# Optimization experiments

Hardware: AMD Instinct MI355X
Metric: run time of the kernel (lower is better)

## Reference

```python
import jax, jax.numpy as jnp
import numpy as np
import math

B, L, OBS, ACT = 2, 1024, 64, 16
OE, AE, RE, TE = 512, 256, 128, 128
C, H, NL, FF = 1024, 16, 4, 4096
DH = C // H


def setup_inputs():
    key = jax.random.key(0)
    ks = jax.random.split(key, 20)
    def nrm(k, shape, std=1.0):
        return jax.random.normal(k, shape, jnp.float32) * std
    kb = jax.random.split(ks[19], 12)
    return {
        'obs_seq': nrm(ks[0], (B, L, OBS)),
        'act_seq': nrm(ks[1], (B, L, ACT)),
        'rew_seq': nrm(ks[2], (B, L, 1)),
        'obs_W': nrm(ks[3], (OBS, OE), OBS ** -0.5), 'obs_b': jnp.zeros((OE,)),
        'act_W': nrm(ks[4], (ACT, AE), ACT ** -0.5), 'act_b': jnp.zeros((AE,)),
        'rew_W': nrm(ks[5], (1, RE), 1.0), 'rew_b': jnp.zeros((RE,)),
        'tr_W': nrm(ks[6], (OBS, TE), OBS ** -0.5), 'tr_b': jnp.zeros((TE,)),
        'bn_gamma': jnp.ones((OBS,)), 'bn_beta': jnp.zeros((OBS,)),
        'ln1_w': jnp.ones((NL, C)), 'ln1_b': jnp.zeros((NL, C)),
        'qkv_W': nrm(kb[0], (NL, C, 3 * C), C ** -0.5), 'qkv_b': jnp.zeros((NL, 3 * C)),
        'out_W': nrm(kb[1], (NL, C, C), C ** -0.5), 'out_b': jnp.zeros((NL, C)),
        'ln2_w': jnp.ones((NL, C)), 'ln2_b': jnp.zeros((NL, C)),
        'fc_W': nrm(kb[2], (NL, C, FF), C ** -0.5), 'fc_b': jnp.zeros((NL, FF)),
        'pj_W': nrm(kb[3], (NL, FF, C), FF ** -0.5), 'pj_b': jnp.zeros((NL, C)),
    }


def _ln(x, w, b):
    m = x.mean(-1, keepdims=True)
    v = ((x - m) ** 2).mean(-1, keepdims=True)
    return (x - m) * jax.lax.rsqrt(v + 1e-5) * w + b


def _forward(obs_seq, act_seq, rew_seq, obs_W, obs_b, act_W, act_b, rew_W, rew_b,
             tr_W, tr_b, bn_gamma, bn_beta, ln1_w, ln1_b, qkv_W, qkv_b, out_W, out_b,
             ln2_w, ln2_b, fc_W, fc_b, pj_W, pj_b):
    # transition branch: prepend first obs, take deltas; BatchNorm1d in training
    # mode uses biased batch stats over (batch, time) per channel.
    full_obs = jnp.concatenate([obs_seq[:, :1], obs_seq], axis=1)  # (B, L+1, OBS)
    obs2 = full_obs[:, :-1]
    tran = full_obs[:, 1:] - full_obs[:, :-1]  # (B, L, OBS)
    tm = tran.mean((0, 1))
    tv = ((tran - tm) ** 2).mean((0, 1))
    tran = (tran - tm) * jax.lax.rsqrt(tv + 1e-5) * bn_gamma + bn_beta
    # encoder_activation is identity
    enc = jnp.concatenate([
        obs2 @ obs_W + obs_b,
        act_seq @ act_W + act_b,
        rew_seq @ rew_W + rew_b,
        tran @ tr_W + tr_b,
    ], axis=-1)  # (B, L, C)
    mask = jnp.tril(jnp.ones((L, L), dtype=bool))

    def block(x, p):
        l1w, l1b, qW, qb, oW, ob, l2w, l2b, fW, fb, pW, pb = p
        h = _ln(x, l1w, l1b)
        q, k, v = jnp.split(h @ qW + qb, 3, axis=-1)
        q, k, v = (t.reshape(B, L, H, DH).transpose(0, 2, 1, 3) for t in (q, k, v))
        s = jnp.einsum('bhqd,bhkd->bhqk', q, k) / math.sqrt(DH)
        s = jnp.where(mask, s, -jnp.inf)
        a = jax.nn.softmax(s, axis=-1)
        o = jnp.einsum('bhqk,bhkd->bhqd', a, v).transpose(0, 2, 1, 3).reshape(B, L, C)
        x = x + o @ oW + ob  # residual + out_proj
        h2 = _ln(x, l2w, l2b)
        x = x + jax.nn.relu(h2 @ fW + fb) @ pW + pb  # MLP residual
        return x, None

    x, _ = jax.lax.scan(block, enc, (ln1_w, ln1_b, qkv_W, qkv_b, out_W, out_b,
                                     ln2_w, ln2_b, fc_W, fc_b, pj_W, pj_b))
    return jnp.tanh(x)


def reference(obs_seq, act_seq, rew_seq, obs_W, obs_b, act_W, act_b, rew_W, rew_b,
              tr_W, tr_b, bn_gamma, bn_beta, ln1_w, ln1_b, qkv_W, qkv_b, out_W, out_b,
              ln2_w, ln2_b, fc_W, fc_b, pj_W, pj_b):
    return _forward(obs_seq, act_seq, rew_seq, obs_W, obs_b, act_W, act_b, rew_W, rew_b,
                    tr_W, tr_b, bn_gamma, bn_beta, ln1_w, ln1_b, qkv_W, qkv_b, out_W, out_b,
                    ln2_w, ln2_b, fc_W, fc_b, pj_W, pj_b)
```

## Files before the change

kernel.cpp:

```cpp
#include <hip/hip_runtime.h>
#include <hip/hip_bf16.h>
#include <math.h>

constexpr int kB   = 2;
constexpr int kL   = 1024;
constexpr int kOBS = 64;
constexpr int kACT = 16;
constexpr int kC   = 1024;
constexpr int kH   = 16;
constexpr int kDH  = 64;
constexpr int kFF  = 4096;
constexpr int kNL  = 4;
constexpr int kRows = kB * kL;
constexpr int kOE = 512, kAE = 256, kRE = 128, kTE = 128;

typedef _Float16 f16x8 __attribute__((ext_vector_type(8)));
typedef _Float16 f16x4 __attribute__((ext_vector_type(4)));
typedef float    f32x4 __attribute__((ext_vector_type(4)));

__device__ __forceinline__ unsigned short f2h(float x) {
    return __builtin_bit_cast(unsigned short, (_Float16)x);
}
__device__ __forceinline__ void gload_lds16(const void* g, void* l) {
    __builtin_amdgcn_global_load_lds(
        (const __attribute__((address_space(1))) unsigned int*)g,
        (__attribute__((address_space(3))) unsigned int*)l, 16, 0, 0);
}

__global__ __launch_bounds__(256) void tran_stats_kernel(
    const float* __restrict__ obs, float* __restrict__ tm, float* __restrict__ tv)
{
    const int f = blockIdx.x;
    const int tid = threadIdx.x;
    float sum = 0.f, sq = 0.f;
    for (int r = tid; r < kRows; r += 256) {
        const int t = r & (kL - 1);
        float d = 0.f;
        if (t > 0) {
            const float cur  = obs[(size_t)r * kOBS + f];
            const float prev = obs[(size_t)(r - 1) * kOBS + f];
            d = cur - prev;
        }
        sum += d; sq += d * d;
    }
    for (int off = 32; off > 0; off >>= 1) {
        sum += __shfl_down(sum, off);
        sq  += __shfl_down(sq, off);
    }
    __shared__ float sa[4], sb[4];
    if ((tid & 63) == 0) { sa[tid >> 6] = sum; sb[tid >> 6] = sq; }
    __syncthreads();
    if (tid == 0) {
        const float ts = sa[0] + sa[1] + sa[2] + sa[3];
        const float tq = sb[0] + sb[1] + sb[2] + sb[3];
        const float m = ts / (float)kRows;
        tm[f] = m;
        tv[f] = tq / (float)kRows - m * m;
    }
}

__global__ __launch_bounds__(256) void encode_kernel(
    const float* __restrict__ obs, const float* __restrict__ act, const float* __restrict__ rew,
    const float* __restrict__ obs_W, const float* __restrict__ obs_b,
    const float* __restrict__ act_W, const float* __restrict__ act_b,
    const float* __restrict__ rew_W, const float* __restrict__ rew_b,
    const float* __restrict__ tr_W,  const float* __restrict__ tr_b,
    const float* __restrict__ bn_g,  const float* __restrict__ bn_b,
    const float* __restrict__ tm,    const float* __restrict__ tv,
    float* __restrict__ enc)
{
    const int row = blockIdx.x;
    const int t = row & (kL - 1);
    const int tid = threadIdx.x;
    __shared__ float s_obs2[kOBS];
    __shared__ float s_tran[kOBS];
    __shared__ float s_act[kACT];
    __shared__ float s_rew;
    if (tid < kOBS) {
        const float cur  = obs[(size_t)row * kOBS + tid];
        const float prev = (t > 0) ? obs[(size_t)(row - 1) * kOBS + tid] : cur;
        s_obs2[tid] = prev;
        const float tr = cur - prev;
        s_tran[tid] = (tr - tm[tid]) * rsqrtf(tv[tid] + 1e-5f) * bn_g[tid] + bn_b[tid];
    } else if (tid < kOBS + kACT) {
        s_act[tid - kOBS] = act[(size_t)row * kACT + (tid - kOBS)];
    } else if (tid == kOBS + kACT) {
        s_rew = rew[row];
    }
    __syncthreads();
    float* er = enc + (size_t)row * kC;
    #pragma unroll
    for (int s = 0; s < 4; ++s) {
        const int c = tid + s * 256;
        float v;
        if (c < kOE) {
            v = obs_b[c];
            #pragma unroll
            for (int k = 0; k < kOBS; ++k) v += s_obs2[k] * obs_W[k * kOE + c];
        } else if (c < kOE + kAE) {
            const int cc = c - kOE;
            v = act_b[cc];
            #pragma unroll
            for (int k = 0; k < kACT; ++k) v += s_act[k] * act_W[k * kAE + cc];
        } else if (c < kOE + kAE + kRE) {
            const int cc = c - (kOE + kAE);
            v = s_rew * rew_W[cc] + rew_b[cc];
        } else {
            const int cc = c - (kOE + kAE + kRE);
            v = tr_b[cc];
            #pragma unroll
            for (int k = 0; k < kOBS; ++k) v += s_tran[k] * tr_W[k * kTE + cc];
        }
        er[c] = v;
    }
}

__global__ __launch_bounds__(256) void ln_kernel(
    const float* __restrict__ x, const float* __restrict__ w,
    const float* __restrict__ b, unsigned short* __restrict__ out)
{
    const int row = blockIdx.x;
    const int tid = threadIdx.x;
    const float4 xv = *reinterpret_cast<const float4*>(&x[(size_t)row * kC + tid * 4]);
    float s = xv.x + xv.y + xv.z + xv.w;
    float q = xv.x * xv.x + xv.y * xv.y + xv.z * xv.z + xv.w * xv.w;
    for (int off = 32; off > 0; off >>= 1) {
        s += __shfl_down(s, off);
        q += __shfl_down(q, off);
    }
    __shared__ float sa[4], sb[4];
    if ((tid & 63) == 0) { sa[tid >> 6] = s; sb[tid >> 6] = q; }
    __syncthreads();
    const float ts = sa[0] + sa[1] + sa[2] + sa[3];
    const float tq = sb[0] + sb[1] + sb[2] + sb[3];
    const float mean = ts * (1.f / kC);
    const float var  = tq * (1.f / kC) - mean * mean;
    const float rstd = rsqrtf(var + 1e-5f);
    const float4 wv = *reinterpret_cast<const float4*>(&w[tid * 4]);
    const float4 bv = *reinterpret_cast<const float4*>(&b[tid * 4]);
    ushort4 o;
    o.x = f2h((xv.x - mean) * rstd * wv.x + bv.x);
    o.y = f2h((xv.y - mean) * rstd * wv.y + bv.y);
    o.z = f2h((xv.z - mean) * rstd * wv.z + bv.z);
    o.w = f2h((xv.w - mean) * rstd * wv.w + bv.w);
    *reinterpret_cast<ushort4*>(&out[(size_t)row * kC + tid * 4]) = o;
}

__device__ __forceinline__ void convT_tile(
    const float* __restrict__ W, unsigned short* __restrict__ WT,
    int K, int N, int k0, int n0, int tid)
{
    __shared__ unsigned short t[64][68];
    const int r = tid >> 4, c4 = (tid & 15) * 4;
    #pragma unroll
    for (int s = 0; s < 4; ++s) {
        const int rr = r + s * 16;
        const float4 v = *reinterpret_cast<const float4*>(&W[(size_t)(k0 + rr) * N + n0 + c4]);
        t[rr][c4 + 0] = f2h(v.x);
        t[rr][c4 + 1] = f2h(v.y);
        t[rr][c4 + 2] = f2h(v.z);
        t[rr][c4 + 3] = f2h(v.w);
    }
    __syncthreads();
    #pragma unroll
    for (int s = 0; s < 4; ++s) {
        const int rn = r + s * 16;
        ushort4 o;
        o.x = t[c4 + 0][rn];
        o.y = t[c4 + 1][rn];
        o.z = t[c4 + 2][rn];
        o.w = t[c4 + 3][rn];
        *reinterpret_cast<ushort4*>(&WT[(size_t)(n0 + rn) * K + k0 + c4]) = o;
    }
}

__global__ __launch_bounds__(256) void convert_layer_kernel(
    const float* __restrict__ qW, const float* __restrict__ oW,
    const float* __restrict__ fW, const float* __restrict__ pW,
    unsigned short* __restrict__ qWT, unsigned short* __restrict__ oWT,
    unsigned short* __restrict__ fWT, unsigned short* __restrict__ pWT)
{
    int bid = blockIdx.x;
    const int tid = threadIdx.x;
    if (bid < 768)  {
        convT_tile(qW, qWT, 1024, 3072, (bid / 48) * 64, (bid % 48) * 64, tid);
    } else if (bid < 1024) {
        bid -= 768;
        convT_tile(oW, oWT, 1024, 1024, (bid / 16) * 64, (bid % 16) * 64, tid);
    } else if (bid < 2048) {
        bid -= 1024;
        convT_tile(fW, fWT, 1024, 4096, (bid / 64) * 64, (bid % 64) * 64, tid);
    } else {
        bid -= 2048;
        convT_tile(pW, pWT, 4096, 1024, (bid / 16) * 64, (bid % 16) * 64, tid);
    }
}

template<int RELU, int RES, int MODE>
__global__ __launch_bounds__(256) void gemm_f16_kernel(
    const unsigned short* __restrict__ A,
    const unsigned short* __restrict__ BT,
    const float* __restrict__ bias,
    float* __restrict__ Cf, unsigned short* __restrict__ Ch,
    unsigned short* __restrict__ Cv,
    int M, int N, int K)
{
    __shared__ __align__(16) unsigned short As[3][128 * 32];
    __shared__ __align__(16) unsigned short Bs[3][128 * 32];
    const int tid = threadIdx.x;
    const int lane = tid & 63;
    const int wv   = tid >> 6;
    const int wr = wv >> 1, wc = wv & 1;

    const int nx  = gridDim.x;
    const int nxy = gridDim.x * gridDim.y;
    int flat = blockIdx.x + nx * blockIdx.y + nxy * blockIdx.z;
    const int cpx = (nxy * gridDim.z) >> 3;
    flat = (flat & 7) * cpx + (flat >> 3);
    const int bx = flat % nx;
    const int by = (flat / nx) % gridDim.y;
    const int bz = flat / nxy;

    const int bm = by * 128;
    const int bn = bx * 128;
    const int ksz  = K / gridDim.z;
    const int kbeg = bz * ksz;
    const int kend = kbeg + ksz;

    const int grow = tid >> 2;
    const int gs   = (tid & 3) ^ ((tid >> 3) & 3);

    const int fr = lane & 15;
    const int kb = lane >> 4;

    auto stage = [&](int k0, int buf) {
        gload_lds16(A  + (size_t)(bm + grow) * K + k0 + gs * 8,
                    (char*)&As[buf][0] + wv * 1024);
        gload_lds16(A  + (size_t)(bm + 64 + grow) * K + k0 + gs * 8,
                    (char*)&As[buf][0] + 4096 + wv * 1024);
        gload_lds16(BT + (size_t)(bn + grow) * K + k0 + gs * 8,
                    (char*)&Bs[buf][0] + wv * 1024);
        gload_lds16(BT + (size_t)(bn + 64 + grow) * K + k0 + gs * 8,
                    (char*)&Bs[buf][0] + 4096 + wv * 1024);
    };

    f32x4 acc[4][4] = {};

    stage(kbeg, 0);
    if (kbeg + 32 < kend) stage(kbeg + 32, 1);
    int cur = 0;
    for (int k0 = kbeg; k0 < kend; k0 += 32) {
        if (k0 + 32 < kend) {
            asm volatile("s_waitcnt vmcnt(4)" ::: "memory");
        } else {
            asm volatile("s_waitcnt vmcnt(0)" ::: "memory");
        }
        asm volatile("s_waitcnt lgkmcnt(0)" ::: "memory");
        __builtin_amdgcn_sched_barrier(0);
        __builtin_amdgcn_s_barrier();
        __builtin_amdgcn_sched_barrier(0);

        f16x8 a[4], b[4];
        #pragma unroll
        for (int m = 0; m < 4; ++m) {
            const int row = wr * 64 + m * 16 + fr;
            a[m] = *reinterpret_cast<const f16x8*>(
                &As[cur][row * 32 + ((kb ^ ((row >> 1) & 3)) * 8)]);
        }
        #pragma unroll
        for (int n = 0; n < 4; ++n) {
            const int row = wc * 64 + n * 16 + fr;
            b[n] = *reinterpret_cast<const f16x8*>(
                &Bs[cur][row * 32 + ((kb ^ ((row >> 1) & 3)) * 8)]);
        }
        if (k0 + 64 < kend) {
            int sb = cur + 2; if (sb >= 3) sb -= 3;
            stage(k0 + 64, sb);
        }
        #pragma unroll
        for (int m = 0; m < 4; ++m)
            #pragma unroll
            for (int n = 0; n < 4; ++n)
                acc[m][n] = __builtin_amdgcn_mfma_f32_16x16x32_f16(
                    a[m], b[n], acc[m][n], 0, 0, 0);

        ++cur; if (cur >= 3) cur = 0;
    }

    const int fq = lane >> 4;
    if (MODE == 4) {
        const bool addb = (bz == 0);
        #pragma unroll
        for (int n = 0; n < 4; ++n) {
            const int c = bn + wc * 64 + n * 16 + fr;
            const float bv = addb ? bias[c] : 0.f;
            #pragma unroll
            for (int m = 0; m < 4; ++m) {
                #pragma unroll
                for (int j = 0; j < 4; ++j) {
                    const int r = bm + wr * 64 + m * 16 + fq * 4 + j;
                    atomicAdd(&Cf[(size_t)r * N + c], acc[m][n][j] + bv);
                }
            }
        }
        return;
    }
    if (MODE == 2) {
        if (bn < 2 * kC) {
            #pragma unroll
            for (int n = 0; n < 4; ++n) {
                const int c = bn + wc * 64 + n * 16 + fr;
                const float bv = bias[c];
                #pragma unroll
                for (int m = 0; m < 4; ++m) {
                    #pragma unroll
                    for (int j = 0; j < 4; ++j) {
                        const int r = bm + wr * 64 + m * 16 + fq * 4 + j;
                        Ch[(size_t)r * (2 * kC) + c] = f2h(acc[m][n][j] + bv);
                    }
                }
            }
        } else {
            #pragma unroll
            for (int n = 0; n < 4; ++n) {
                const int c  = bn + wc * 64 + n * 16 + fr;
                const int cc = c - 2 * kC;
                const int hh = cc >> 6, dd = cc & 63;
                const float bv = bias[c];
                #pragma unroll
                for (int m = 0; m < 4; ++m) {
                    const int rr = bm + wr * 64 + m * 16 + fq * 4;
                    const int bb = rr >> 10, t0 = rr & 1023;
                    f16x4 pk;
                    #pragma unroll
                    for (int j = 0; j < 4; ++j) pk[j] = (_Float16)(acc[m][n][j] + bv);
                    *reinterpret_cast<f16x4*>(
                        &Cv[((size_t)(bb * kH + hh) * kDH + dd) * kL + t0]) = pk;
                }
            }
        }
        return;
    }
    #pragma unroll
    for (int n = 0; n < 4; ++n) {
        const int c = bn + wc * 64 + n * 16 + fr;
        const float bv = bias[c];
        #pragma unroll
        for (int m = 0; m < 4; ++m) {
            #pragma unroll
            for (int j = 0; j < 4; ++j) {
                const int r = bm + wr * 64 + m * 16 + fq * 4 + j;
                float v = acc[m][n][j] + bv;
                if (RES)  v += Cf[(size_t)r * N + c];
                if (RELU) v = fmaxf(v, 0.f);
                if (MODE == 1) Ch[(size_t)r * N + c] = f2h(v);
                else           Cf[(size_t)r * N + c] = v;
            }
        }
    }
}

__device__ __forceinline__ int swz(int row, int slot) {
    return row * 64 + ((slot ^ (row & 7)) * 8);
}

__global__ __launch_bounds__(256) void attn_mfma_kernel(
    const unsigned short* __restrict__ qk,
    const unsigned short* __restrict__ vt,
    unsigned short* __restrict__ o)
{
    const int bid = blockIdx.x;
    const int bh  = bid & 31;
    const int qb  = ((bid >> 5) + bh) & 15;
    const int b   = bh >> 4;
    const int h   = bh & 15;
    const int tid  = threadIdx.x;
    const int lane = tid & 63;
    const int wv   = tid >> 6;
    const int fr = lane & 15;
    const int g  = lane >> 4;

    __shared__ __align__(16) unsigned short Qs[64 * 64];
    __shared__ __align__(16) unsigned short Ks[64 * 64];
    __shared__ __align__(16) unsigned short Vts[64 * 64];
    __shared__ __align__(16) unsigned short Ps[64 * 64];

    const int qlo = qb * 64;

    {
        const int r = tid >> 2, s = tid & 3;
        const unsigned short* qg = &qk[(size_t)(b * kL + qlo + r) * (2 * kC) + h * kDH];
        f16x8 v0 = *reinterpret_cast<const f16x8*>(&qg[s * 8]);
        f16x8 v1 = *reinterpret_cast<const f16x8*>(&qg[(s + 4) * 8]);
        #pragma unroll
        for (int i = 0; i < 8; ++i) { v0[i] *= (_Float16)0.125f; v1[i] *= (_Float16)0.125f; }
        *reinterpret_cast<f16x8*>(&Qs[swz(r, s)])     = v0;
        *reinterpret_cast<f16x8*>(&Qs[swz(r, s + 4)]) = v1;
    }
    __syncthreads();

    f16x8 qfrag[2];
    #pragma unroll
    for (int kf = 0; kf < 2; ++kf)
        qfrag[kf] = *reinterpret_cast<const f16x8*>(&Qs[swz(wv * 16 + fr, kf * 4 + g)]);

    float m = -INFINITY, l = 0.f;
    f32x4 acc_o[4] = {};
    const int qg_row = qlo + wv * 16 + fr;

    for (int k0 = 0; k0 <= qlo; k0 += 64) {
        __syncthreads();
        {
            const int r = tid >> 2, s = tid & 3;
            const unsigned short* kg = &qk[(size_t)(b * kL + k0 + r) * (2 * kC) + kC + h * kDH];
            *reinterpret_cast<f16x8*>(&Ks[swz(r, s)])     = *reinterpret_cast<const f16x8*>(&kg[s * 8]);
            *reinterpret_cast<f16x8*>(&Ks[swz(r, s + 4)]) = *reinterpret_cast<const f16x8*>(&kg[(s + 4) * 8]);
            const unsigned short* vg = &vt[((size_t)(b * kH + h) * kDH + r) * kL + k0];
            *reinterpret_cast<f16x8*>(&Vts[swz(r, s)])     = *reinterpret_cast<const f16x8*>(&vg[s * 8]);
            *reinterpret_cast<f16x8*>(&Vts[swz(r, s + 4)]) = *reinterpret_cast<const f16x8*>(&vg[(s + 4) * 8]);
        }
        __syncthreads();

        f32x4 acc_s[4] = {};
        #pragma unroll
        for (int kf = 0; kf < 2; ++kf) {
            const f16x8 qf = qfrag[kf];
            #pragma unroll
            for (int n = 0; n < 4; ++n) {
                const f16x8 kfr = *reinterpret_cast<const f16x8*>(&Ks[swz(n * 16 + fr, kf * 4 + g)]);
                acc_s[n] = __builtin_amdgcn_mfma_f32_16x16x32_f16(kfr, qf, acc_s[n], 0, 0, 0);
            }
        }

        if (k0 == qlo) {
            #pragma unroll
            for (int n = 0; n < 4; ++n)
                #pragma unroll
                for (int j = 0; j < 4; ++j)
                    if (k0 + n * 16 + g * 4 + j > qg_row) acc_s[n][j] = -INFINITY;
        }

        float mx = -INFINITY;
        #pragma unroll
        for (int n = 0; n < 4; ++n)
            #pragma unroll
            for (int j = 0; j < 4; ++j) mx = fmaxf(mx, acc_s[n][j]);
        mx = fmaxf(mx, __shfl_xor(mx, 16));
        mx = fmaxf(mx, __shfl_xor(mx, 32));
        const float mn  = fmaxf(m, mx);
        const float fac = __expf(m - mn);
        float p[4][4];
        float psum = 0.f;
        #pragma unroll
        for (int n = 0; n < 4; ++n)
            #pragma unroll
            for (int j = 0; j < 4; ++j) { p[n][j] = __expf(acc_s[n][j] - mn); psum += p[n][j]; }
        psum += __shfl_xor(psum, 16);
        psum += __shfl_xor(psum, 32);
        l = l * fac + psum;
        m = mn;
        #pragma unroll
        for (int dt = 0; dt < 4; ++dt)
            #pragma unroll
            for (int j = 0; j < 4; ++j) acc_o[dt][j] *= fac;

        #pragma unroll
        for (int n = 0; n < 4; ++n) {
            f16x4 pk;
            #pragma unroll
            for (int j = 0; j < 4; ++j) pk[j] = (_Float16)p[n][j];
            *reinterpret_cast<f16x4*>(&Ps[swz(wv * 16 + fr, 2 * n + (g >> 1)) + (g & 1) * 4]) = pk;
        }

        #pragma unroll
        for (int kf = 0; kf < 2; ++kf) {
            const f16x8 pf = *reinterpret_cast<const f16x8*>(&Ps[swz(wv * 16 + fr, kf * 4 + g)]);
            #pragma unroll
            for (int dt = 0; dt < 4; ++dt) {
                const f16x8 vf = *reinterpret_cast<const f16x8*>(&Vts[swz(dt * 16 + fr, kf * 4 + g)]);
                acc_o[dt] = __builtin_amdgcn_mfma_f32_16x16x32_f16(vf, pf, acc_o[dt], 0, 0, 0);
            }
        }
    }

    const float rl = 1.f / l;
    unsigned short* ob = &o[(size_t)(b * kL + qg_row) * kC + h * kDH];
    #pragma unroll
    for (int dt = 0; dt < 4; ++dt) {
        f16x4 pk;
        #pragma unroll
        for (int j = 0; j < 4; ++j) pk[j] = (_Float16)(acc_o[dt][j] * rl);
        *reinterpret_cast<f16x4*>(&ob[dt * 16 + g * 4]) = pk;
    }
}

__global__ __launch_bounds__(256) void tanh_kernel(float* __restrict__ x)
{
    const size_t i = ((size_t)blockIdx.x * 256 + threadIdx.x) * 4;
    float4 v = *reinterpret_cast<float4*>(&x[i]);
    v.x = tanhf(v.x); v.y = tanhf(v.y); v.z = tanhf(v.z); v.w = tanhf(v.w);
    *reinterpret_cast<float4*>(&x[i]) = v;
}

extern "C" void kernel_launch(void* const* d_in, const int* in_sizes, int n_in,
                              void* d_out, int out_size, void* d_ws, size_t ws_size,
                              hipStream_t stream)
{
    (void)in_sizes; (void)n_in; (void)out_size; (void)ws_size;
    const float* obs    = (const float*)d_in[0];
    const float* act    = (const float*)d_in[1];
    const float* rew    = (const float*)d_in[2];
    const float* obs_W  = (const float*)d_in[3];
    const float* obs_b  = (const float*)d_in[4];
    const float* act_W  = (const float*)d_in[5];
    const float* act_b  = (const float*)d_in[6];
    const float* rew_W  = (const float*)d_in[7];
    const float* rew_b  = (const float*)d_in[8];
    const float* tr_W   = (const float*)d_in[9];
    const float* tr_b   = (const float*)d_in[10];
    const float* bn_g   = (const float*)d_in[11];
    const float* bn_b   = (const float*)d_in[12];
    const float* ln1_w  = (const float*)d_in[13];
    const float* ln1_b  = (const float*)d_in[14];
    const float* qkv_W  = (const float*)d_in[15];
    const float* qkv_b  = (const float*)d_in[16];
    const float* out_W  = (const float*)d_in[17];
    const float* out_b  = (const float*)d_in[18];
    const float* ln2_w  = (const float*)d_in[19];
    const float* ln2_b  = (const float*)d_in[20];
    const float* fc_W   = (const float*)d_in[21];
    const float* fc_b   = (const float*)d_in[22];
    const float* pj_W   = (const float*)d_in[23];
    const float* pj_b   = (const float*)d_in[24];

    float* x  = (float*)d_out;
    float* ws = (float*)d_ws;
    float* tm   = ws;
    float* tv   = ws + 64;
    unsigned short* wbuf  = (unsigned short*)(ws + 128);
    unsigned short* h_hf  = wbuf + 12582912;
    unsigned short* ao_hf = h_hf + (size_t)kRows * kC;
    unsigned short* ff_hf = ao_hf + (size_t)kRows * kC;
    unsigned short* qk_hf = ff_hf + (size_t)kRows * kFF;
    unsigned short* vt_hf = qk_hf + (size_t)kRows * 2 * kC;
    unsigned short* qWT = wbuf;
    unsigned short* oWT = qWT + 3 * kC * kC;
    unsigned short* fWT = oWT + kC * kC;
    unsigned short* pWT = fWT + kC * kFF;

    tran_stats_kernel<<<kOBS, 256, 0, stream>>>(obs, tm, tv);
    encode_kernel<<<kRows, 256, 0, stream>>>(obs, act, rew,
        obs_W, obs_b, act_W, act_b, rew_W, rew_b, tr_W, tr_b, bn_g, bn_b, tm, tv, x);

    for (int lyr = 0; lyr < kNL; ++lyr) {
        const float* qW = qkv_W + (size_t)lyr * kC * 3 * kC;
        const float* qB = qkv_b + (size_t)lyr * 3 * kC;
        const float* oW = out_W + (size_t)lyr * kC * kC;
        const float* oB = out_b + (size_t)lyr * kC;
        const float* fW = fc_W + (size_t)lyr * kC * kFF;
        const float* fB = fc_b + (size_t)lyr * kFF;
        const float* pW = pj_W + (size_t)lyr * kFF * kC;
        const float* pB = pj_b + (size_t)lyr * kC;

        convert_layer_kernel<<<3072, 256, 0, stream>>>(
            qW, oW, fW, pW, qWT, oWT, fWT, pWT);

        ln_kernel<<<kRows, 256, 0, stream>>>(x, ln1_w + lyr * kC, ln1_b + lyr * kC, h_hf);
        gemm_f16_kernel<0,0,2><<<dim3(3 * kC / 128, kRows / 128), 256, 0, stream>>>(
            h_hf, qWT, qB, nullptr, qk_hf, vt_hf, kRows, 3 * kC, kC);
        attn_mfma_kernel<<<dim3(512), 256, 0, stream>>>(qk_hf, vt_hf, ao_hf);
        gemm_f16_kernel<0,0,4><<<dim3(kC / 128, kRows / 128, 4), 256, 0, stream>>>(
            ao_hf, oWT, oB, x, nullptr, nullptr, kRows, kC, kC);
        ln_kernel<<<kRows, 256, 0, stream>>>(x, ln2_w + lyr * kC, ln2_b + lyr * kC, h_hf);
        gemm_f16_kernel<1,0,1><<<dim3(kFF / 128, kRows / 128), 256, 0, stream>>>(
            h_hf, fWT, fB, nullptr, ff_hf, nullptr, kRows, kFF, kC);
        gemm_f16_kernel<0,0,4><<<dim3(kC / 128, kRows / 128, 4), 256, 0, stream>>>(
            ff_hf, pWT, pB, x, nullptr, nullptr, kRows, kC, kFF);
    }
    tanh_kernel<<<kRows * kC / 1024, 256, 0, stream>>>(x);
}
```

Measured before the change: 690.2 us.

## Load attention Q/K/V fragments directly from global and raise proj split-K

The attention kernel no longer stages Q, K and V^T tiles in shared memory. Each wave now loads its MFMA fragments straight from global memory, which removes both per-iteration __syncthreads and the LDS round trip. The cost is that the four waves in a block each read the same K/V tile, so the kernel leans on L1/L2 to absorb that redundant traffic. Separately, the MLP down-projection GEMM grid goes from 4 to 8 K-splits to raise parallelism, at the price of more atomic or partial-sum accumulation into x.

```diff
diff --git a/kernel.cpp b/kernel.cpp
--- a/kernel.cpp
+++ b/kernel.cpp
@@ -380,55 +380,38 @@
     const int fr = lane & 15;
     const int g  = lane >> 4;
 
-    __shared__ __align__(16) unsigned short Qs[64 * 64];
-    __shared__ __align__(16) unsigned short Ks[64 * 64];
-    __shared__ __align__(16) unsigned short Vts[64 * 64];
     __shared__ __align__(16) unsigned short Ps[64 * 64];
 
     const int qlo = qb * 64;
-
+    const int qg_row = qlo + wv * 16 + fr;
+
+    f16x8 qfrag[2];
     {
-        const int r = tid >> 2, s = tid & 3;
-        const unsigned short* qg = &qk[(size_t)(b * kL + qlo + r) * (2 * kC) + h * kDH];
-        f16x8 v0 = *reinterpret_cast<const f16x8*>(&qg[s * 8]);
-        f16x8 v1 = *reinterpret_cast<const f16x8*>(&qg[(s + 4) * 8]);
-        #pragma unroll
-        for (int i = 0; i < 8; ++i) { v0[i] *= (_Float16)0.125f; v1[i] *= (_Float16)0.125f; }
-        *reinterpret_cast<f16x8*>(&Qs[swz(r, s)])     = v0;
-        *reinterpret_cast<f16x8*>(&Qs[swz(r, s + 4)]) = v1;
-    }
-    __syncthreads();
-
-    f16x8 qfrag[2];
-    #pragma unroll
-    for (int kf = 0; kf < 2; ++kf)
-        qfrag[kf] = *reinterpret_cast<const f16x8*>(&Qs[swz(wv * 16 + fr, kf * 4 + g)]);
+        const unsigned short* qg = &qk[(size_t)(b * kL + qg_row) * (2 * kC) + h * kDH];
+        #pragma unroll
+        for (int kf = 0; kf < 2; ++kf) {
+            f16x8 v = *reinterpret_cast<const f16x8*>(&qg[(kf * 4 + g) * 8]);
+            #pragma unroll
+            for (int i = 0; i < 8; ++i) v[i] *= (_Float16)0.125f;
+            qfrag[kf] = v;
+        }
+    }
 
     float m = -INFINITY, l = 0.f;
     f32x4 acc_o[4] = {};
-    const int qg_row = qlo + wv * 16 + fr;
+
+    const unsigned short* kbase = &qk[(size_t)(b * kL) * (2 * kC) + kC + h * kDH];
+    const unsigned short* vbase = &vt[(size_t)(b * kH + h) * kDH * kL];
 
     for (int k0 = 0; k0 <= qlo; k0 += 64) {
-        __syncthreads();
-        {
-            const int r = tid >> 2, s = tid & 3;
-            const unsigned short* kg = &qk[(size_t)(b * kL + k0 + r) * (2 * kC) + kC + h * kDH];
-            *reinterpret_cast<f16x8*>(&Ks[swz(r, s)])     = *reinterpret_cast<const f16x8*>(&kg[s * 8]);
-            *reinterpret_cast<f16x8*>(&Ks[swz(r, s + 4)]) = *reinterpret_cast<const f16x8*>(&kg[(s + 4) * 8]);
-            const unsigned short* vg = &vt[((size_t)(b * kH + h) * kDH + r) * kL + k0];
-            *reinterpret_cast<f16x8*>(&Vts[swz(r, s)])     = *reinterpret_cast<const f16x8*>(&vg[s * 8]);
-            *reinterpret_cast<f16x8*>(&Vts[swz(r, s + 4)]) = *reinterpret_cast<const f16x8*>(&vg[(s + 4) * 8]);
-        }
-        __syncthreads();
-
         f32x4 acc_s[4] = {};
         #pragma unroll
         for (int kf = 0; kf < 2; ++kf) {
-            const f16x8 qf = qfrag[kf];
             #pragma unroll
             for (int n = 0; n < 4; ++n) {
-                const f16x8 kfr = *reinterpret_cast<const f16x8*>(&Ks[swz(n * 16 + fr, kf * 4 + g)]);
-                acc_s[n] = __builtin_amdgcn_mfma_f32_16x16x32_f16(kfr, qf, acc_s[n], 0, 0, 0);
+                const f16x8 kfr = *reinterpret_cast<const f16x8*>(
+                    &kbase[(size_t)(k0 + n * 16 + fr) * (2 * kC) + (kf * 4 + g) * 8]);
+                acc_s[n] = __builtin_amdgcn_mfma_f32_16x16x32_f16(kfr, qfrag[kf], acc_s[n], 0, 0, 0);
             }
         }
 
@@ -477,7 +460,8 @@
             const f16x8 pf = *reinterpret_cast<const f16x8*>(&Ps[swz(wv * 16 + fr, kf * 4 + g)]);
             #pragma unroll
             for (int dt = 0; dt < 4; ++dt) {
-                const f16x8 vf = *reinterpret_cast<const f16x8*>(&Vts[swz(dt * 16 + fr, kf * 4 + g)]);
+                const f16x8 vf = *reinterpret_cast<const f16x8*>(
+                    &vbase[(size_t)(dt * 16 + fr) * kL + k0 + (kf * 4 + g) * 8]);
                 acc_o[dt] = __builtin_amdgcn_mfma_f32_16x16x32_f16(vf, pf, acc_o[dt], 0, 0, 0);
             }
         }
@@ -574,7 +558,7 @@
         ln_kernel<<<kRows, 256, 0, stream>>>(x, ln2_w + lyr * kC, ln2_b + lyr * kC, h_hf);
         gemm_f16_kernel<1,0,1><<<dim3(kFF / 128, kRows / 128), 256, 0, stream>>>(
             h_hf, fWT, fB, nullptr, ff_hf, nullptr, kRows, kFF, kC);
-        gemm_f16_kernel<0,0,4><<<dim3(kC / 128, kRows / 128, 4), 256, 0, stream>>>(
+        gemm_f16_kernel<0,0,4><<<dim3(kC / 128, kRows / 128, 8), 256, 0, stream>>>(
             ff_hf, pWT, pB, x, nullptr, nullptr, kRows, kC, kFF);
     }
     tanh_kernel<<<kRows * kC / 1024, 256, 0, stream>>>(x);
```

Result: slower. 870.9 us (+26.2%).
